# Optimization experiments

Measured on AMD Instinct MI355X. Metric: run time of the kernel, lower is better.

The kernel has to match this reference:

```python
import jax, jax.numpy as jnp
import numpy as np

B = 64
C = 384
HEADS = 6
HD = 64
MLP = 1536
LAYERS = 12
PATCH = 16
IMG = 224
GRID = IMG // PATCH  # 14
NPATCH = GRID * GRID  # 196
NCLS = 100
EPS = 1e-6
PRUNE = {2: 0.1, 4: 0.15, 6: 0.2}
SCALE = HD ** -0.5


def layer_norm(x, g, b):
    m = jnp.mean(x, axis=-1, keepdims=True)
    v = jnp.var(x, axis=-1, keepdims=True)
    return (x - m) * jax.lax.rsqrt(v + EPS) * g + b


def attention(x, qkv_w, qkv_b, proj_w, proj_b):
    # x: [B, N, C]; weights stored as [in, out]
    Bn, N, _ = x.shape
    qkv = x @ qkv_w + qkv_b                      # [B, N, 3C]
    qkv = qkv.reshape(Bn, N, 3, HEADS, HD).transpose(2, 0, 3, 1, 4)
    q, k, v = qkv[0], qkv[1], qkv[2]             # [B, H, N, HD]
    attn = jax.nn.softmax(jnp.einsum('bhnd,bhmd->bhnm', q, k) * SCALE, axis=-1)
    out = jnp.einsum('bhnm,bhmd->bhnd', attn, v)
    out = out.transpose(0, 2, 1, 3).reshape(Bn, N, C)
    return out @ proj_w + proj_b, attn


def mlp(x, fc1_w, fc1_b, fc2_w, fc2_b):
    h = jax.nn.gelu(x @ fc1_w + fc1_b, approximate=False)
    return h @ fc2_w + fc2_b


def prune(x, attn, ratio):
    # x: [B, N, C]; attn: [B, H, N, N]
    scores = attn[:, :, 0, 1:].mean(axis=1)      # CLS attention to tokens, head-avg [B, N-1]
    keep = int(scores.shape[1] * (1 - ratio))
    _, idx = jax.lax.top_k(scores, keep)         # [B, keep], descending score order (matches torch.topk)
    tokens = jnp.take_along_axis(x[:, 1:, :], idx[:, :, None], axis=1)
    return jnp.concatenate([x[:, :1, :], tokens], axis=1)


def patch_embed(x, patch_w, patch_b):
    # 16x16 stride-16 conv == patchify + matmul. x: [B, 3, 224, 224]
    Bn = x.shape[0]
    p = x.reshape(Bn, 3, GRID, PATCH, GRID, PATCH).transpose(0, 2, 4, 1, 3, 5)
    p = p.reshape(Bn, NPATCH, 3 * PATCH * PATCH)
    return p @ patch_w + patch_b


def setup_inputs() -> dict:
    key = jax.random.key(0)
    ks = jax.random.split(key, 10)
    s = 0.02
    d = {}
    d['x'] = jax.random.normal(ks[0], (B, 3, IMG, IMG), jnp.float32)
    d['patch_w'] = jax.random.normal(ks[1], (3 * PATCH * PATCH, C), jnp.float32) * s
    d['patch_b'] = jnp.zeros((C,), jnp.float32)
    d['cls_token'] = jax.random.normal(ks[2], (1, 1, C), jnp.float32) * s
    d['pos_embed'] = jax.random.normal(ks[3], (1, NPATCH + 1, C), jnp.float32) * s
    d['ln1_g'] = jnp.ones((LAYERS, C), jnp.float32)
    d['ln1_b'] = jnp.zeros((LAYERS, C), jnp.float32)
    d['qkv_w'] = jax.random.normal(ks[4], (LAYERS, C, 3 * C), jnp.float32) * s
    d['qkv_b'] = jnp.zeros((LAYERS, 3 * C), jnp.float32)
    d['proj_w'] = jax.random.normal(ks[5], (LAYERS, C, C), jnp.float32) * s
    d['proj_b'] = jnp.zeros((LAYERS, C), jnp.float32)
    d['ln2_g'] = jnp.ones((LAYERS, C), jnp.float32)
    d['ln2_b'] = jnp.zeros((LAYERS, C), jnp.float32)
    d['fc1_w'] = jax.random.normal(ks[6], (LAYERS, C, MLP), jnp.float32) * s
    d['fc1_b'] = jnp.zeros((LAYERS, MLP), jnp.float32)
    d['fc2_w'] = jax.random.normal(ks[7], (LAYERS, MLP, C), jnp.float32) * s
    d['fc2_b'] = jnp.zeros((LAYERS, C), jnp.float32)
    d['norm_g'] = jnp.ones((C,), jnp.float32)
    d['norm_b'] = jnp.zeros((C,), jnp.float32)
    d['head_w'] = jax.random.normal(ks[8], (C, NCLS), jnp.float32) * s
    d['head_b'] = jnp.zeros((NCLS,), jnp.float32)
    return d


def reference(x, patch_w, patch_b, cls_token, pos_embed, ln1_g, ln1_b, qkv_w, qkv_b,
              proj_w, proj_b, ln2_g, ln2_b, fc1_w, fc1_b, fc2_w, fc2_b,
              norm_g, norm_b, head_w, head_b):
    Bn = x.shape[0]
    h = patch_embed(x, patch_w, patch_b)                          # [B, 196, C]
    cls = jnp.broadcast_to(cls_token, (Bn, 1, C))
    h = jnp.concatenate([cls, h], axis=1) + pos_embed             # [B, 197, C]
    for i in range(LAYERS):
        y, attn = attention(layer_norm(h, ln1_g[i], ln1_b[i]),
                            qkv_w[i], qkv_b[i], proj_w[i], proj_b[i])
        h = h + y
        if i in PRUNE:
            h = prune(h, attn, PRUNE[i])
        h = h + mlp(layer_norm(h, ln2_g[i], ln2_b[i]),
                    fc1_w[i], fc1_b[i], fc2_w[i], fc2_b[i])
    h = layer_norm(h, norm_g, norm_b)
    return h[:, 0] @ head_w + head_b                              # [B, NCLS]
```

## Files before the change

kernel.cpp:

```cpp
#include <hip/hip_runtime.h>
#include <hip/hip_bf16.h>
#include <math.h>

#define BATCH 64
#define CDIM 384
#define NHEADS 6
#define HD 64
#define MLPD 1536
#define NLAYERS 12
#define NPATCH 196
#define NTOK0 197
#define NCLS 100

typedef unsigned short ushortT;
typedef __attribute__((ext_vector_type(8))) short short8v;
typedef __attribute__((ext_vector_type(4))) float float4v;

__device__ inline ushortT f2b(float f) {
  union { float f; unsigned u; } x; x.f = f;
  unsigned r = x.u + 0x7fffu + ((x.u >> 16) & 1u);
  return (ushortT)(r >> 16);
}
__device__ inline float b2f(ushortT u) {
  union { unsigned u; float f; } x; x.u = ((unsigned)u) << 16;
  return x.f;
}

__device__ inline void gload_lds16(const ushortT* g, ushortT* l) {
  __builtin_amdgcn_global_load_lds((const __attribute__((address_space(1))) void*)g,
                                   (__attribute__((address_space(3))) void*)l, 16, 0, 0);
}

__device__ inline float wave_sum(float v) {
  #pragma unroll
  for (int o = 32; o > 0; o >>= 1) v += __shfl_xor(v, o);
  return v;
}

__global__ __launch_bounds__(256) void im2col_bf16(const float* __restrict__ x, ushortT* __restrict__ P) {
  int i = blockIdx.x * 256 + threadIdx.x;
  const int total = BATCH * NPATCH * 768;
  if (i >= total) return;
  int k = i % 768;
  int row = i / 768;
  int c = k >> 8;
  int r = k & 255;
  int py = r >> 4, px = r & 15;
  int b = row / NPATCH;
  int p = row % NPATCH;
  int gy = p / 14, gx = p % 14;
  P[i] = f2b(x[(((size_t)b * 3 + c) * 224 + gy * 16 + py) * 224 + gx * 16 + px]);
}

__global__ __launch_bounds__(256) void assemble_kernel(const float* __restrict__ patchout,
                                                       const float* __restrict__ cls_tok,
                                                       const float* __restrict__ pos,
                                                       float* __restrict__ h) {
  int i = blockIdx.x * 256 + threadIdx.x;
  const int total = BATCH * NTOK0 * CDIM;
  if (i >= total) return;
  int c = i % CDIM;
  int n = (i / CDIM) % NTOK0;
  int b = i / (CDIM * NTOK0);
  float v = (n == 0) ? cls_tok[c] : patchout[((size_t)b * NPATCH + (n - 1)) * CDIM + c];
  h[i] = v + pos[n * CDIM + c];
}

__global__ __launch_bounds__(256) void wtrans_layer(const float* __restrict__ qkv_w, const float* __restrict__ proj_w,
                                                    const float* __restrict__ fc1_w, const float* __restrict__ fc2_w,
                                                    ushortT* __restrict__ wq, ushortT* __restrict__ wp,
                                                    ushortT* __restrict__ w1, ushortT* __restrict__ w2) {
  int id = blockIdx.x;
  const float* W; ushortT* O; int K, N, t;
  if (id < 432)       { W = qkv_w; O = wq; K = 384;  N = 1152; t = id; }
  else if (id < 576)  { W = proj_w; O = wp; K = 384; N = 384;  t = id - 432; }
  else if (id < 1152) { W = fc1_w; O = w1; K = 384;  N = 1536; t = id - 576; }
  else                { W = fc2_w; O = w2; K = 1536; N = 384;  t = id - 1152; }
  int tilesK = K >> 5;
  int k0 = (t % tilesK) << 5, n0 = (t / tilesK) << 5;
  __shared__ float tile[32][33];
  int tx = threadIdx.x & 31, ty = threadIdx.x >> 5;
  #pragma unroll
  for (int i = 0; i < 4; ++i)
    tile[ty + 8 * i][tx] = W[(size_t)(k0 + ty + 8 * i) * N + n0 + tx];
  __syncthreads();
  #pragma unroll
  for (int i = 0; i < 4; ++i)
    O[(size_t)(n0 + ty + 8 * i) * K + k0 + tx] = f2b(tile[tx][ty + 8 * i]);
}

__global__ __launch_bounds__(256) void wtrans_one(const float* __restrict__ W, ushortT* __restrict__ O, int K, int N) {
  int t = blockIdx.x;
  int tilesK = K >> 5;
  int k0 = (t % tilesK) << 5, n0 = (t / tilesK) << 5;
  __shared__ float tile[32][33];
  int tx = threadIdx.x & 31, ty = threadIdx.x >> 5;
  #pragma unroll
  for (int i = 0; i < 4; ++i)
    tile[ty + 8 * i][tx] = W[(size_t)(k0 + ty + 8 * i) * N + n0 + tx];
  __syncthreads();
  #pragma unroll
  for (int i = 0; i < 4; ++i)
    O[(size_t)(n0 + ty + 8 * i) * K + k0 + tx] = f2b(tile[tx][ty + 8 * i]);
}

template<int ACT, int RES, int OBF>
__global__ __launch_bounds__(256) void gemm_mfma(const ushortT* __restrict__ A, const ushortT* __restrict__ Wt,
                                                 const float* __restrict__ bias, const float* __restrict__ res,
                                                 void* __restrict__ outp, int M, int N, int K, int gx) {
  __shared__ __align__(16) ushortT Asl[2][4096];
  __shared__ __align__(16) ushortT Bsl[2][4096];
  const int tid = threadIdx.x;
  const int lane = tid & 63, wave = tid >> 6;
  const int wr = wave >> 1, wc = wave & 1;

  const int nwg = gridDim.x;
  const int orig = blockIdx.x;
  const int q = nwg >> 3, r = nwg & 7;
  const int xcd = orig & 7;
  const int wgid = (xcd < r ? xcd * (q + 1) : r * (q + 1) + (xcd - r) * q) + (orig >> 3);
  const int bm = (wgid / gx) * 128, bn = (wgid % gx) * 128;

  float4v acc[4][4] = {};

  const int srow = wave * 16 + (lane >> 2);
  const int scol = (lane & 3) * 8;
  const ushortT* ag0 = A + (size_t)(bm + srow) * K + scol;
  const ushortT* ag1 = A + (size_t)(bm + 64 + srow) * K + scol;
  const ushortT* bg0 = Wt + (size_t)(bn + srow) * K + scol;
  const ushortT* bg1 = Wt + (size_t)(bn + 64 + srow) * K + scol;

  const int fr = lane & 15, g8 = (lane >> 4) * 8;
  const int nt = K >> 5;

  gload_lds16(ag0, &Asl[0][wave * 512]);
  gload_lds16(ag1, &Asl[0][2048 + wave * 512]);
  gload_lds16(bg0, &Bsl[0][wave * 512]);
  gload_lds16(bg1, &Bsl[0][2048 + wave * 512]);
  __syncthreads();

  int cur = 0;
  for (int t = 0; t < nt; ++t) {
    if (t + 1 < nt) {
      const int k0 = (t + 1) << 5;
      const int nxt = cur ^ 1;
      gload_lds16(ag0 + k0, &Asl[nxt][wave * 512]);
      gload_lds16(ag1 + k0, &Asl[nxt][2048 + wave * 512]);
      gload_lds16(bg0 + k0, &Bsl[nxt][wave * 512]);
      gload_lds16(bg1 + k0, &Bsl[nxt][2048 + wave * 512]);
    }
    short8v af[4], bf[4];
    #pragma unroll
    for (int i = 0; i < 4; ++i) {
      af[i] = *(const short8v*)&Asl[cur][(wr * 64 + i * 16 + fr) * 32 + g8];
      bf[i] = *(const short8v*)&Bsl[cur][(wc * 64 + i * 16 + fr) * 32 + g8];
    }
    #pragma unroll
    for (int i = 0; i < 4; ++i)
      #pragma unroll
      for (int j = 0; j < 4; ++j)
        acc[i][j] = __builtin_amdgcn_mfma_f32_16x16x32_bf16(af[i], bf[j], acc[i][j], 0, 0, 0);
    if (t + 1 < nt) {
      __syncthreads();
      cur ^= 1;
    }
  }

  const int c0 = lane & 15;
  const int r4 = (lane >> 4) * 4;
  #pragma unroll
  for (int i = 0; i < 4; ++i) {
    #pragma unroll
    for (int j = 0; j < 4; ++j) {
      const int col = bn + wc * 64 + j * 16 + c0;
      #pragma unroll
      for (int qq = 0; qq < 4; ++qq) {
        const int row = bm + wr * 64 + i * 16 + r4 + qq;
        if (row < M) {
          float v = acc[i][j][qq] + bias[col];
          if (ACT == 1) v = 0.5f * v * (1.0f + erff(v * 0.70710678118654752f));
          if (RES) v += res[(size_t)row * N + col];
          if (OBF) ((ushortT*)outp)[(size_t)row * N + col] = f2b(v);
          else     ((float*)outp)[(size_t)row * N + col] = v;
        }
      }
    }
  }
}

__global__ __launch_bounds__(256) void ln_bf16(const float* __restrict__ in, ushortT* __restrict__ out,
                                               const float* __restrict__ g, const float* __restrict__ bb,
                                               int rows) {
  const int r = blockIdx.x * 4 + (threadIdx.x >> 6);
  if (r >= rows) return;
  const int t = threadIdx.x & 63;
  const float* xr = in + (size_t)r * CDIM;
  ushortT* orow = out + (size_t)r * CDIM;
  float v[6];
  float s = 0.f;
  #pragma unroll
  for (int i = 0; i < 6; ++i) { v[i] = xr[i * 64 + t]; s += v[i]; }
  s = wave_sum(s);
  float mean = s * (1.0f / CDIM);
  float q = 0.f;
  #pragma unroll
  for (int i = 0; i < 6; ++i) { float d = v[i] - mean; q += d * d; }
  q = wave_sum(q);
  float rstd = rsqrtf(q * (1.0f / CDIM) + 1e-6f);
  #pragma unroll
  for (int i = 0; i < 6; ++i) {
    int c = i * 64 + t;
    orow[c] = f2b((v[i] - mean) * rstd * g[c] + bb[c]);
  }
}

__global__ __launch_bounds__(64) void ln_kernel(const float* __restrict__ in, float* __restrict__ out,
                                                const float* __restrict__ g, const float* __restrict__ bb,
                                                int rows, size_t in_stride, size_t out_stride) {
  int r = blockIdx.x;
  if (r >= rows) return;
  const float* xr = in + (size_t)r * in_stride;
  float* orow = out + (size_t)r * out_stride;
  int t = threadIdx.x;
  float v[6];
  float s = 0.f;
  #pragma unroll
  for (int i = 0; i < 6; ++i) { v[i] = xr[i * 64 + t]; s += v[i]; }
  s = wave_sum(s);
  float mean = s * (1.0f / CDIM);
  float q = 0.f;
  #pragma unroll
  for (int i = 0; i < 6; ++i) { float d = v[i] - mean; q += d * d; }
  q = wave_sum(q);
  float rstd = rsqrtf(q * (1.0f / CDIM) + 1e-6f);
  #pragma unroll
  for (int i = 0; i < 6; ++i) {
    int c = i * 64 + t;
    orow[c] = (v[i] - mean) * rstd * g[c] + bb[c];
  }
}

template<int KS>
__global__ __launch_bounds__(256) void attn3(const ushortT* __restrict__ qkv, ushortT* __restrict__ attnout,
                                             float* __restrict__ cls_attn, int N) {
  constexpr int NT = 2 * KS;
  constexpr int KT = 32 * KS;
  const int h = blockIdx.y, b = blockIdx.z;
  const int rb = blockIdx.x * 64;
  const int tid = threadIdx.x;
  const int w = tid >> 6, l = tid & 63;
  const int c = l & 15, g = l >> 4;

  __shared__ __align__(16) ushortT Vt[64][232];
  __shared__ __align__(16) ushortT Ps[4][16][232];

  const ushortT* bq = qkv + (size_t)(b * N) * 1152 + (size_t)h * 64;

  {
    const int vr = tid >> 3, vc = (tid & 7) * 8;
    for (int p = 0; p < KT; p += 32) {
      const int m = vr + p;
      if (m < N) {
        short8v v8 = *(const short8v*)(bq + (size_t)m * 1152 + 768 + vc);
        #pragma unroll
        for (int j = 0; j < 8; ++j) Vt[vc + j][m] = (ushortT)v8[j];
      } else if (m < KT) {
        #pragma unroll
        for (int j = 0; j < 8; ++j) Vt[vc + j][m] = 0;
      }
    }
  }
  __syncthreads();

  short8v qf0, qf1;
  {
    int row = rb + 16 * w + c; if (row >= N) row = N - 1;
    const ushortT* qrow = bq + (size_t)row * 1152;
    qf0 = *(const short8v*)(qrow + g * 8);
    qf1 = *(const short8v*)(qrow + 32 + g * 8);
  }

  float4v sc[NT];
  #pragma unroll
  for (int kt = 0; kt < NT; ++kt) {
    int krow = 16 * kt + c; if (krow >= N) krow = N - 1;
    const ushortT* kr = bq + (size_t)krow * 1152 + 384;
    short8v b0 = *(const short8v*)(kr + g * 8);
    short8v b1 = *(const short8v*)(kr + 32 + g * 8);
    float4v a = {};
    a = __builtin_amdgcn_mfma_f32_16x16x32_bf16(qf0, b0, a, 0, 0, 0);
    a = __builtin_amdgcn_mfma_f32_16x16x32_bf16(qf1, b1, a, 0, 0, 0);
    sc[kt] = a;
  }

  float m4[4] = {-INFINITY, -INFINITY, -INFINITY, -INFINITY};
  #pragma unroll
  for (int kt = 0; kt < NT; ++kt) {
    const bool valid = (16 * kt + c) < N;
    #pragma unroll
    for (int q = 0; q < 4; ++q) {
      float s = valid ? sc[kt][q] * 0.125f : -INFINITY;
      sc[kt][q] = s;
      m4[q] = fmaxf(m4[q], s);
    }
  }
  #pragma unroll
  for (int q = 0; q < 4; ++q) {
    #pragma unroll
    for (int o = 1; o <= 8; o <<= 1) m4[q] = fmaxf(m4[q], __shfl_xor(m4[q], o));
  }
  float sum4[4] = {0.f, 0.f, 0.f, 0.f};
  #pragma unroll
  for (int kt = 0; kt < NT; ++kt) {
    #pragma unroll
    for (int q = 0; q < 4; ++q) {
      float e = __expf(sc[kt][q] - m4[q]);
      sc[kt][q] = e;
      sum4[q] += e;
    }
  }
  #pragma unroll
  for (int q = 0; q < 4; ++q) {
    #pragma unroll
    for (int o = 1; o <= 8; o <<= 1) sum4[q] += __shfl_xor(sum4[q], o);
  }
  float inv4[4];
  #pragma unroll
  for (int q = 0; q < 4; ++q) inv4[q] = 1.0f / sum4[q];

  #pragma unroll
  for (int kt = 0; kt < NT; ++kt) {
    #pragma unroll
    for (int q = 0; q < 4; ++q) Ps[w][4 * g + q][16 * kt + c] = f2b(sc[kt][q]);
  }

  if (rb == 0 && w == 0 && g == 0) {
    const float inv0 = inv4[0];
    #pragma unroll
    for (int kt = 0; kt < NT; ++kt) {
      const int col = 16 * kt + c;
      if (col >= 1 && col < N)
        cls_attn[((size_t)b * NHEADS + h) * (N - 1) + (col - 1)] = sc[kt][0] * inv0;
    }
  }

  float4v oacc[4] = {};
  #pragma unroll
  for (int s2 = 0; s2 < KS; ++s2) {
    short8v pa = *(const short8v*)&Ps[w][c][32 * s2 + 8 * g];
    #pragma unroll
    for (int nt = 0; nt < 4; ++nt) {
      short8v vb = *(const short8v*)&Vt[16 * nt + c][32 * s2 + 8 * g];
      oacc[nt] = __builtin_amdgcn_mfma_f32_16x16x32_bf16(pa, vb, oacc[nt], 0, 0, 0);
    }
  }

  #pragma unroll
  for (int nt = 0; nt < 4; ++nt) {
    #pragma unroll
    for (int q = 0; q < 4; ++q) {
      const int row = rb + 16 * w + 4 * g + q;
      if (row < N)
        attnout[((size_t)(b * N + row)) * CDIM + h * 64 + 16 * nt + c] = f2b(oacc[nt][q] * inv4[q]);
    }
  }
}

__global__ __launch_bounds__(256) void topk_rank(const float* __restrict__ cls_attn, int* __restrict__ idx,
                                                 int Nm1, int Kkeep) {
  const int b = blockIdx.x;
  const int t = threadIdx.x;
  __shared__ float s_sc[224];
  if (t < Nm1) {
    const float* ca = cls_attn + (size_t)b * NHEADS * Nm1 + t;
    float s = 0.f;
    #pragma unroll
    for (int h = 0; h < NHEADS; ++h) s += ca[h * Nm1];
    s_sc[t] = s * (1.0f / NHEADS);
  }
  __syncthreads();
  if (t < Nm1) {
    const float mys = s_sc[t];
    int r = 0;
    for (int i = 0; i < Nm1; ++i) {
      float si = s_sc[i];
      r += (si > mys || (si == mys && i < t)) ? 1 : 0;
    }
    if (r < Kkeep) idx[b * Kkeep + r] = t;
  }
}

__global__ __launch_bounds__(256) void gather_kernel(const float* __restrict__ h, const int* __restrict__ idx,
                                                     float* __restrict__ outb, int N, int Kkeep) {
  size_t total = (size_t)BATCH * (1 + Kkeep) * CDIM;
  size_t i = (size_t)blockIdx.x * 256 + threadIdx.x;
  if (i >= total) return;
  int c = (int)(i % CDIM);
  size_t r = i / CDIM;
  int n = (int)(r % (1 + Kkeep));
  int b = (int)(r / (1 + Kkeep));
  int src = (n == 0) ? 0 : 1 + idx[b * Kkeep + (n - 1)];
  outb[i] = h[((size_t)b * N + src) * CDIM + c];
}

__global__ __launch_bounds__(256) void gemm_f32(const float* __restrict__ A, const float* __restrict__ W,
                                                const float* __restrict__ bias, float* __restrict__ out,
                                                int M, int N, int K) {
  __shared__ __align__(16) float As[16][64];
  __shared__ __align__(16) float Ws[16][64];
  const int tid = threadIdx.x;
  const int tx = tid & 15, ty = tid >> 4;
  const int bm = blockIdx.y * 64, bn = blockIdx.x * 64;
  float acc[4][4] = {};
  const int ma = tid >> 2;
  const int ka = (tid & 3) << 2;
  const int kw = ty;
  const int nw = tx << 2;
  for (int k0 = 0; k0 < K; k0 += 16) {
    {
      float4 a4 = make_float4(0.f, 0.f, 0.f, 0.f);
      if (bm + ma < M) a4 = *reinterpret_cast<const float4*>(&A[(size_t)(bm + ma) * K + k0 + ka]);
      As[ka + 0][ma] = a4.x; As[ka + 1][ma] = a4.y; As[ka + 2][ma] = a4.z; As[ka + 3][ma] = a4.w;
    }
    {
      const int gn = bn + nw;
      const float* wp = &W[(size_t)(k0 + kw) * N + gn];
      #pragma unroll
      for (int j = 0; j < 4; ++j) Ws[kw][nw + j] = (gn + j < N) ? wp[j] : 0.f;
    }
    __syncthreads();
    #pragma unroll
    for (int kk = 0; kk < 16; ++kk) {
      float4 a = *reinterpret_cast<const float4*>(&As[kk][ty << 2]);
      float4 w = *reinterpret_cast<const float4*>(&Ws[kk][tx << 2]);
      float av[4] = {a.x, a.y, a.z, a.w};
      float wv[4] = {w.x, w.y, w.z, w.w};
      #pragma unroll
      for (int i = 0; i < 4; ++i)
        #pragma unroll
        for (int j = 0; j < 4; ++j)
          acc[i][j] = fmaf(av[i], wv[j], acc[i][j]);
    }
    __syncthreads();
  }
  #pragma unroll
  for (int i = 0; i < 4; ++i) {
    int r = bm + (ty << 2) + i;
    if (r >= M) continue;
    #pragma unroll
    for (int j = 0; j < 4; ++j) {
      int cidx = bn + (tx << 2) + j;
      if (cidx >= N) continue;
      out[(size_t)r * N + cidx] = acc[i][j] + bias[cidx];
    }
  }
}

extern "C" void kernel_launch(void* const* d_in, const int* in_sizes, int n_in,
                              void* d_out, int out_size, void* d_ws, size_t ws_size,
                              hipStream_t stream) {
  const float* x        = (const float*)d_in[0];
  const float* patch_w  = (const float*)d_in[1];
  const float* patch_b  = (const float*)d_in[2];
  const float* cls_tok  = (const float*)d_in[3];
  const float* pos      = (const float*)d_in[4];
  const float* ln1_g    = (const float*)d_in[5];
  const float* ln1_b    = (const float*)d_in[6];
  const float* qkv_w    = (const float*)d_in[7];
  const float* qkv_b    = (const float*)d_in[8];
  const float* proj_w   = (const float*)d_in[9];
  const float* proj_b   = (const float*)d_in[10];
  const float* ln2_g    = (const float*)d_in[11];
  const float* ln2_b    = (const float*)d_in[12];
  const float* fc1_w    = (const float*)d_in[13];
  const float* fc1_b    = (const float*)d_in[14];
  const float* fc2_w    = (const float*)d_in[15];
  const float* fc2_b    = (const float*)d_in[16];
  const float* norm_g   = (const float*)d_in[17];
  const float* norm_b   = (const float*)d_in[18];
  const float* head_w   = (const float*)d_in[19];
  const float* head_b   = (const float*)d_in[20];
  float* out = (float*)d_out;

  float* ws = (float*)d_ws;
  float* hA       = ws;
  float* big      = ws + 4841472;
  ushortT* big_u  = (ushortT*)big;
  float* patchout = big + 4816896;
  float* hB       = ws + 14524416;
  ushortT* lnb_u  = (ushortT*)(ws + 19365888);
  ushortT* attn_u = (ushortT*)(ws + 21786624);
  ushortT* wbuf_u = (ushortT*)(ws + 24207360);
  float* cls_attn = ws + 25092096;
  int*   idxbuf   = (int*)(ws + 25179904);
  float* cls0     = ws + 25191168;

  ushortT* wq = wbuf_u;
  ushortT* wp = wbuf_u + 442368;
  ushortT* w1 = wbuf_u + 589824;
  ushortT* w2 = wbuf_u + 1179648;

  {
    int total = BATCH * NPATCH * 768;
    im2col_bf16<<<(total + 255) / 256, 256, 0, stream>>>(x, big_u);
    wtrans_one<<<288, 256, 0, stream>>>(patch_w, wbuf_u, 768, CDIM);
    gemm_mfma<0, 0, 0><<<3 * 98, 256, 0, stream>>>(big_u, wbuf_u, patch_b, nullptr, patchout,
                                                   BATCH * NPATCH, CDIM, 768, 3);
    int tot2 = BATCH * NTOK0 * CDIM;
    assemble_kernel<<<(tot2 + 255) / 256, 256, 0, stream>>>(patchout, cls_tok, pos, hA);
  }

  float* h = hA;
  float* hOther = hB;
  int ncur = NTOK0;
  for (int i = 0; i < NLAYERS; ++i) {
    int M = BATCH * ncur;
    int gy = (M + 127) / 128;
    wtrans_layer<<<1728, 256, 0, stream>>>(qkv_w + (size_t)i * CDIM * 3 * CDIM,
                                           proj_w + (size_t)i * CDIM * CDIM,
                                           fc1_w + (size_t)i * CDIM * MLPD,
                                           fc2_w + (size_t)i * MLPD * CDIM,
                                           wq, wp, w1, w2);
    ln_bf16<<<(M + 3) / 4, 256, 0, stream>>>(h, lnb_u, ln1_g + i * CDIM, ln1_b + i * CDIM, M);
    gemm_mfma<0, 0, 1><<<9 * gy, 256, 0, stream>>>(lnb_u, wq, qkv_b + i * 3 * CDIM, nullptr,
                                                   big_u, M, 3 * CDIM, CDIM, 9);
    {
      dim3 g((ncur + 63) / 64, NHEADS, BATCH);
      int ks = (ncur + 31) / 32;
      if (ks == 7)      attn3<7><<<g, 256, 0, stream>>>(big_u, attn_u, cls_attn, ncur);
      else if (ks == 6) attn3<6><<<g, 256, 0, stream>>>(big_u, attn_u, cls_attn, ncur);
      else if (ks == 5) attn3<5><<<g, 256, 0, stream>>>(big_u, attn_u, cls_attn, ncur);
      else              attn3<4><<<g, 256, 0, stream>>>(big_u, attn_u, cls_attn, ncur);
    }
    gemm_mfma<0, 1, 0><<<3 * gy, 256, 0, stream>>>(attn_u, wp, proj_b + i * CDIM, h,
                                                   h, M, CDIM, CDIM, 3);
    if (i == 2 || i == 4 || i == 6) {
      int keep = (i == 2) ? 176 : (i == 4) ? 149 : 119;
      int Nm1 = ncur - 1;
      topk_rank<<<BATCH, 256, 0, stream>>>(cls_attn, idxbuf, Nm1, keep);
      int newN = 1 + keep;
      size_t gtot = (size_t)BATCH * newN * CDIM;
      gather_kernel<<<(int)((gtot + 255) / 256), 256, 0, stream>>>(h, idxbuf, hOther, ncur, keep);
      float* tmp = h; h = hOther; hOther = tmp;
      ncur = newN;
      M = BATCH * ncur;
      gy = (M + 127) / 128;
    }
    ln_bf16<<<(M + 3) / 4, 256, 0, stream>>>(h, lnb_u, ln2_g + i * CDIM, ln2_b + i * CDIM, M);
    gemm_mfma<1, 0, 1><<<12 * gy, 256, 0, stream>>>(lnb_u, w1, fc1_b + i * MLPD, nullptr,
                                                    big_u, M, MLPD, CDIM, 12);
    gemm_mfma<0, 1, 0><<<3 * gy, 256, 0, stream>>>(big_u, w2, fc2_b + i * CDIM, h,
                                                   h, M, CDIM, MLPD, 3);
  }

  ln_kernel<<<BATCH, 64, 0, stream>>>(h, cls0, norm_g, norm_b, BATCH, (size_t)ncur * CDIM, CDIM);
  gemm_f32<<<dim3(2, 1), 256, 0, stream>>>(cls0, head_w, head_b, out, BATCH, NCLS, CDIM);
}
```

Measured before the change: 2.451 ms.

## Triple-buffer GEMM LDS tiles with explicit vmcnt waits and split barriers

Moves the MFMA GEMM from a double-buffered LDS pipeline to a three-stage ring, prefetching tiles three steps ahead. Explicit s_waitcnt vmcnt counts let each iteration wait only for its own tile's loads rather than all outstanding ones. A second barrier after the fragments are read lets the buffer be refilled before the MFMAs run, so global loads overlap compute for longer. The cost is 50% more LDS per block, which may lower occupancy, and the hand-written wait counts assume each step issues exactly four loads and that K is at least three tiles.

```diff
diff --git a/kernel.cpp b/kernel.cpp
--- a/kernel.cpp
+++ b/kernel.cpp
@@ -108,8 +108,8 @@
 __global__ __launch_bounds__(256) void gemm_mfma(const ushortT* __restrict__ A, const ushortT* __restrict__ Wt,
                                                  const float* __restrict__ bias, const float* __restrict__ res,
                                                  void* __restrict__ outp, int M, int N, int K, int gx) {
-  __shared__ __align__(16) ushortT Asl[2][4096];
-  __shared__ __align__(16) ushortT Bsl[2][4096];
+  __shared__ __align__(16) ushortT Asl[3][4096];
+  __shared__ __align__(16) ushortT Bsl[3][4096];
   const int tid = threadIdx.x;
   const int lane = tid & 63, wave = tid >> 6;
   const int wr = wave >> 1, wc = wave & 1;
@@ -133,37 +133,49 @@
   const int fr = lane & 15, g8 = (lane >> 4) * 8;
   const int nt = K >> 5;
 
-  gload_lds16(ag0, &Asl[0][wave * 512]);
-  gload_lds16(ag1, &Asl[0][2048 + wave * 512]);
-  gload_lds16(bg0, &Bsl[0][wave * 512]);
-  gload_lds16(bg1, &Bsl[0][2048 + wave * 512]);
-  __syncthreads();
-
-  int cur = 0;
+  #pragma unroll
+  for (int t = 0; t < 3; ++t) {
+    const int k0 = t << 5;
+    gload_lds16(ag0 + k0, &Asl[t][wave * 512]);
+    gload_lds16(ag1 + k0, &Asl[t][2048 + wave * 512]);
+    gload_lds16(bg0 + k0, &Bsl[t][wave * 512]);
+    gload_lds16(bg1 + k0, &Bsl[t][2048 + wave * 512]);
+  }
+
+  int bufi = 0;
   for (int t = 0; t < nt; ++t) {
-    if (t + 1 < nt) {
-      const int k0 = (t + 1) << 5;
-      const int nxt = cur ^ 1;
-      gload_lds16(ag0 + k0, &Asl[nxt][wave * 512]);
-      gload_lds16(ag1 + k0, &Asl[nxt][2048 + wave * 512]);
-      gload_lds16(bg0 + k0, &Bsl[nxt][wave * 512]);
-      gload_lds16(bg1 + k0, &Bsl[nxt][2048 + wave * 512]);
-    }
+    if (t < nt - 2)      asm volatile("s_waitcnt vmcnt(8)" ::: "memory");
+    else if (t == nt - 2) asm volatile("s_waitcnt vmcnt(4)" ::: "memory");
+    else                  asm volatile("s_waitcnt vmcnt(0)" ::: "memory");
+    __builtin_amdgcn_s_barrier();
+
+    const ushortT* As_ = &Asl[bufi][0];
+    const ushortT* Bs_ = &Bsl[bufi][0];
     short8v af[4], bf[4];
     #pragma unroll
     for (int i = 0; i < 4; ++i) {
-      af[i] = *(const short8v*)&Asl[cur][(wr * 64 + i * 16 + fr) * 32 + g8];
-      bf[i] = *(const short8v*)&Bsl[cur][(wc * 64 + i * 16 + fr) * 32 + g8];
-    }
+      af[i] = *(const short8v*)&As_[(wr * 64 + i * 16 + fr) * 32 + g8];
+      bf[i] = *(const short8v*)&Bs_[(wc * 64 + i * 16 + fr) * 32 + g8];
+    }
+    asm volatile("s_waitcnt lgkmcnt(0)" ::: "memory");
+    __builtin_amdgcn_sched_barrier(0);
+    __builtin_amdgcn_s_barrier();
+
+    if (t + 3 < nt) {
+      const int k0 = (t + 3) << 5;
+      gload_lds16(ag0 + k0, &Asl[bufi][wave * 512]);
+      gload_lds16(ag1 + k0, &Asl[bufi][2048 + wave * 512]);
+      gload_lds16(bg0 + k0, &Bsl[bufi][wave * 512]);
+      gload_lds16(bg1 + k0, &Bsl[bufi][2048 + wave * 512]);
+    }
+
     #pragma unroll
     for (int i = 0; i < 4; ++i)
       #pragma unroll
       for (int j = 0; j < 4; ++j)
         acc[i][j] = __builtin_amdgcn_mfma_f32_16x16x32_bf16(af[i], bf[j], acc[i][j], 0, 0, 0);
-    if (t + 1 < nt) {
-      __syncthreads();
-      cur ^= 1;
-    }
+
+    bufi = bufi + 1; if (bufi == 3) bufi = 0;
   }
 
   const int c0 = lane & 15;
```

After: 2.496 ms. No clear change (+1.8%).
